# Optimization experiments

Hardware: AMD Instinct MI355X
Metric: run time of the kernel (lower is better)

## Reference

```python
import jax, jax.numpy as jnp
import numpy as np

HEADS = 16
DIM_HEAD = 64
SCALE = DIM_HEAD ** -0.5


def setup_inputs() -> dict:
    key = jax.random.key(0)
    k1, k2, k3, k4 = jax.random.split(key, 4)
    dim = 1024
    inner = HEADS * DIM_HEAD  # 1024
    b, n = 4, 2048
    x = jax.random.normal(k1, (b, n, dim), dtype=jnp.float32)
    # weights stored as [in, out] (equivalent math to torch Linear)
    w_qkv = jax.random.normal(k2, (dim, inner * 3), dtype=jnp.float32) * (dim ** -0.5)
    w_out = jax.random.normal(k3, (inner, dim), dtype=jnp.float32) * (inner ** -0.5)
    b_out = jax.random.normal(k4, (dim,), dtype=jnp.float32) * 0.01
    return {"x": x, "w_qkv": w_qkv, "w_out": w_out, "b_out": b_out}


def reference(x, w_qkv, w_out, b_out):
    b, n, dim = x.shape
    qkv = x @ w_qkv                                   # [b, n, 3*inner]
    q, k, v = jnp.split(qkv, 3, axis=-1)
    def to_heads(t):
        return t.reshape(b, n, HEADS, DIM_HEAD).transpose(0, 2, 1, 3)  # b h n d
    q, k, v = to_heads(q) * SCALE, to_heads(k), to_heads(v)
    dots = jnp.einsum('bhid,bhjd->bhij', q, k)        # [b, h, n, n]
    mask_value = -jnp.finfo(dots.dtype).max
    causal_mask = jnp.triu(jnp.ones((n, n), dtype=bool), k=1)
    dots = jnp.where(causal_mask, mask_value, dots)
    attn = jax.nn.softmax(dots, axis=-1)
    out = jnp.einsum('bhij,bhjd->bhid', attn, v)      # [b, h, n, d]
    out = out.transpose(0, 2, 1, 3).reshape(b, n, HEADS * DIM_HEAD)
    return out @ w_out + b_out
```

## Files before the change

kernel.cpp:

```cpp
#include <hip/hip_runtime.h>
#include <hip/hip_bf16.h>
#include <stdint.h>

typedef __attribute__((ext_vector_type(8))) short bf16x8;
typedef __attribute__((ext_vector_type(4))) float f32x4;
typedef __attribute__((ext_vector_type(4))) unsigned int uint32x4;

#define TOKENS 8192
#define DMODEL 1024
#define NQKV   3072
#define NSEQ   2048
#define NHEAD  16
#define DHEAD  64

__device__ __forceinline__ ushort f32_bf16(float f) {
    uint32_t u = __builtin_bit_cast(uint32_t, f);
    u = (u + 0x7fffu + ((u >> 16) & 1u)) >> 16;
    return (ushort)u;
}

__device__ __forceinline__ unsigned int cvt_pk_bf16(float lo, float hi) {
    unsigned int r;
    asm("v_cvt_pk_bf16_f32 %0, %1, %2" : "=v"(r) : "v"(lo), "v"(hi));
    return r;
}
__device__ __forceinline__ void permlane32_swap(unsigned int& a, unsigned int& b) {
    asm("v_permlane32_swap_b32 %0, %1" : "+v"(a), "+v"(b));
}
__device__ __forceinline__ void permlane16_swap(unsigned int& a, unsigned int& b) {
    asm("v_permlane16_swap_b32 %0, %1" : "+v"(a), "+v"(b));
}
__device__ __forceinline__ unsigned opaque_copy(unsigned x) {
    unsigned y;
    asm("v_mov_b32 %0, %1" : "=v"(y) : "v"(x));
    return y;
}

__device__ __forceinline__ float red_max_g(float x) {
    unsigned a = __builtin_bit_cast(unsigned, x);
    unsigned b = opaque_copy(a);
    permlane16_swap(a, b);
    float r = fmaxf(__builtin_bit_cast(float, a), __builtin_bit_cast(float, b));
    unsigned c = __builtin_bit_cast(unsigned, r);
    unsigned d = opaque_copy(c);
    permlane32_swap(c, d);
    return fmaxf(__builtin_bit_cast(float, c), __builtin_bit_cast(float, d));
}
__device__ __forceinline__ float red_sum_g(float x) {
    unsigned a = __builtin_bit_cast(unsigned, x);
    unsigned b = opaque_copy(a);
    permlane16_swap(a, b);
    float r = __builtin_bit_cast(float, a) + __builtin_bit_cast(float, b);
    unsigned c = __builtin_bit_cast(unsigned, r);
    unsigned d = opaque_copy(c);
    permlane32_swap(c, d);
    return __builtin_bit_cast(float, c) + __builtin_bit_cast(float, d);
}

__device__ __forceinline__ void gload16(const void* g, void* l) {
    __builtin_amdgcn_global_load_lds(
        (const __attribute__((address_space(1))) void*)g,
        (__attribute__((address_space(3))) void*)l, 16, 0, 0);
}

__device__ __forceinline__ void barf() {
    asm volatile("" ::: "memory");
    __builtin_amdgcn_s_barrier();
    asm volatile("" ::: "memory");
}

__global__ __launch_bounds__(256) void fused_cvt_kernel(
    const float* __restrict__ x,     ushort* __restrict__ xb,
    const float* __restrict__ wqkv,  ushort* __restrict__ wqkv_t,
    const float* __restrict__ wout,  ushort* __restrict__ wout_t)
{
    __shared__ float tile[64][65];
    const int bid = blockIdx.x;
    const int tid = threadIdx.x;

    if (bid < 8192) {
        const int i = bid * 256 + tid;
        float4 v = reinterpret_cast<const float4*>(x)[i];
        ushort4 o;
        o.x = f32_bf16(v.x); o.y = f32_bf16(v.y);
        o.z = f32_bf16(v.z); o.w = f32_bf16(v.w);
        reinterpret_cast<ushort4*>(xb)[i] = o;
        return;
    }

    const float* w; ushort* wt; int N, bx, by;
    if (bid < 8960) {
        const int r = bid - 8192;
        w = wqkv; wt = wqkv_t; N = NQKV;
        bx = r % 48; by = r / 48;
    } else {
        const int r = bid - 8960;
        w = wout; wt = wout_t; N = DMODEL;
        bx = r % 16; by = r / 16;
    }
    const int rr = tid >> 4;
    const int c4 = (tid & 15) * 4;
    const int n0 = bx * 64;
    const int k0 = by * 64;
    #pragma unroll
    for (int i = 0; i < 4; ++i) {
        const float4 v = *reinterpret_cast<const float4*>(&w[(size_t)(k0 + rr + i * 16) * N + n0 + c4]);
        tile[rr + i * 16][c4 + 0] = v.x;
        tile[rr + i * 16][c4 + 1] = v.y;
        tile[rr + i * 16][c4 + 2] = v.z;
        tile[rr + i * 16][c4 + 3] = v.w;
    }
    __syncthreads();
    #pragma unroll
    for (int i = 0; i < 4; ++i) {
        ushort4 o;
        o.x = f32_bf16(tile[c4 + 0][rr + i * 16]);
        o.y = f32_bf16(tile[c4 + 1][rr + i * 16]);
        o.z = f32_bf16(tile[c4 + 2][rr + i * 16]);
        o.w = f32_bf16(tile[c4 + 3][rr + i * 16]);
        *reinterpret_cast<ushort4*>(&wt[(size_t)(n0 + rr + i * 16) * 1024 + k0 + c4]) = o;
    }
}

template<int MODE, int NX>
__global__ __launch_bounds__(256) void gemm_bt(
    const ushort* __restrict__ A, const ushort* __restrict__ Bt,
    ushort* __restrict__ Qb, ushort* __restrict__ Kb, ushort* __restrict__ Vtb,
    float* __restrict__ Out, const float* __restrict__ bias)
{
    constexpr int K = 1024;
    __shared__ __align__(16) ushort As[2][128 * 32];
    __shared__ __align__(16) ushort Bs[2][128 * 32];

    const int lane = threadIdx.x & 63;
    const int w    = threadIdx.x >> 6;
    const int l16  = lane & 15;
    const int g    = lane >> 4;

    const int nwg  = (int)gridDim.x;
    const int chunk = nwg >> 3;
    const int swz  = (blockIdx.x & 7) * chunk + ((int)blockIdx.x >> 3);
    const int row0 = (swz / NX) * 128;
    const int col0 = (swz % NX) * 128;

    const int wr   = (w >> 1) * 64;
    const int wc   = (w & 1) * 64;

    const int srow  = w * 16 + (lane >> 2);
    const int sswz8 = ((lane & 3) ^ ((lane >> 3) & 3)) * 8;
    const ushort* Ag = A  + (size_t)(row0 + srow) * K + sswz8;
    const ushort* Bg = Bt + (size_t)(col0 + srow) * K + sswz8;
    const int woff = w * (16 * 32);

    const int cq8 = (g ^ ((l16 >> 1) & 3)) * 8;

    f32x4 acc[4][4] = {};

#define GSTAGE(BUF, KK) do {                                             \
        gload16(Ag + (KK),          &As[BUF][woff]);                     \
        gload16(Ag + 64 * K + (KK), &As[BUF][woff + 64 * 32]);           \
        gload16(Bg + (KK),          &Bs[BUF][woff]);                     \
        gload16(Bg + 64 * K + (KK), &Bs[BUF][woff + 64 * 32]);           \
    } while (0)

#define GCOMPUTE(BUF) do {                                               \
        bf16x8 a[4], b[4];                                               \
        _Pragma("unroll")                                                \
        for (int m = 0; m < 4; ++m)                                      \
            a[m] = *reinterpret_cast<const bf16x8*>(                     \
                &As[BUF][(wr + m * 16 + l16) * 32 + cq8]);               \
        _Pragma("unroll")                                                \
        for (int n = 0; n < 4; ++n)                                      \
            b[n] = *reinterpret_cast<const bf16x8*>(                     \
                &Bs[BUF][(wc + n * 16 + l16) * 32 + cq8]);               \
        _Pragma("unroll")                                                \
        for (int m = 0; m < 4; ++m)                                      \
            _Pragma("unroll")                                            \
            for (int n = 0; n < 4; ++n)                                  \
                acc[m][n] = __builtin_amdgcn_mfma_f32_16x16x32_bf16(     \
                    a[m], b[n], acc[m][n], 0, 0, 0);                     \
    } while (0)

    GSTAGE(0, 0);
    GSTAGE(1, 32);
    for (int kk = 0; kk + 128 <= K; kk += 64) {
        asm volatile("s_waitcnt vmcnt(4)" ::: "memory");
        barf();
        GCOMPUTE(0);
        barf();
        GSTAGE(0, kk + 64);
        asm volatile("s_waitcnt vmcnt(4)" ::: "memory");
        barf();
        GCOMPUTE(1);
        barf();
        GSTAGE(1, kk + 96);
    }
    asm volatile("s_waitcnt vmcnt(4)" ::: "memory");
    barf();
    GCOMPUTE(0);
    asm volatile("s_waitcnt vmcnt(0)" ::: "memory");
    barf();
    GCOMPUTE(1);
#undef GSTAGE
#undef GCOMPUTE

    if (MODE == 0) {
        const int part = col0 >> 10;
        const float QSC = 0.18033688011112042f;
        #pragma unroll
        for (int m = 0; m < 4; ++m) {
            const int trow = row0 + wr + m * 16 + 4 * g;
            #pragma unroll
            for (int n = 0; n < 4; ++n) {
                const int c  = col0 + wc + n * 16 + l16;
                const int cc = c & 1023;
                const int h  = cc >> 6, d = cc & 63;
                #pragma unroll
                for (int jj = 0; jj < 4; ++jj) {
                    const int t  = trow + jj;
                    const int bb = t >> 11, nn = t & 2047;
                    const float v = acc[m][n][jj];
                    const size_t bhid = (size_t)(bb * NHEAD + h);
                    if (part == 0)
                        Qb[(bhid * NSEQ + nn) * DHEAD + d] = f32_bf16(v * QSC);
                    else if (part == 1)
                        Kb[(bhid * NSEQ + nn) * DHEAD + d] = f32_bf16(v);
                    else
                        Vtb[bhid * (NSEQ * DHEAD) + (size_t)(nn >> 5) * (DHEAD * 32)
                            + d * 32 + (nn & 31)] = f32_bf16(v);
                }
            }
        }
    } else {
        #pragma unroll
        for (int m = 0; m < 4; ++m) {
            const int trow = row0 + wr + m * 16 + 4 * g;
            #pragma unroll
            for (int n = 0; n < 4; ++n) {
                const int c = col0 + wc + n * 16 + l16;
                const float bv = bias[c];
                #pragma unroll
                for (int jj = 0; jj < 4; ++jj)
                    Out[(size_t)(trow + jj) * DMODEL + c] = acc[m][n][jj] + bv;
            }
        }
    }
}

__device__ __forceinline__ void attn_qk(
    int kt, int qr0s, int l16, int g,
    const bf16x8 (&kk)[4][2],
    const bf16x8 qf0, const bf16x8 qf1,
    f32x4 (&oacc)[4], float& mrun, float& lsum,
    bf16x8& pf0, bf16x8& pf1)
{
    const f32x4 zero = {};
    f32x4 s[4];
    __builtin_amdgcn_s_setprio(1);
    #pragma unroll
    for (int t = 0; t < 4; ++t) {
        s[t] = __builtin_amdgcn_mfma_f32_16x16x32_bf16(kk[t][0], qf0, zero, 0, 0, 0);
        s[t] = __builtin_amdgcn_mfma_f32_16x16x32_bf16(kk[t][1], qf1, s[t], 0, 0, 0);
    }
    __builtin_amdgcn_s_setprio(0);
    if (kt + 63 > qr0s) {
        const int kb = kt + 4 * g - (qr0s + l16);
        #pragma unroll
        for (int t = 0; t < 4; ++t)
            #pragma unroll
            for (int jj = 0; jj < 4; ++jj)
                if (kb + 16 * t + jj > 0) s[t][jj] = -1e30f;
    }
    const float m0 = fmaxf(fmaxf(s[0][0], s[0][1]), s[0][2]);
    const float m1 = fmaxf(fmaxf(s[0][3], s[1][0]), s[1][1]);
    const float m2 = fmaxf(fmaxf(s[1][2], s[1][3]), s[2][0]);
    const float m3 = fmaxf(fmaxf(s[2][1], s[2][2]), s[2][3]);
    const float m4 = fmaxf(fmaxf(s[3][0], s[3][1]), s[3][2]);
    const float m5 = fmaxf(fmaxf(m0, m1), m2);
    const float m6 = fmaxf(fmaxf(m3, m4), s[3][3]);
    const float mxl = fmaxf(m5, m6);
    if (__any(mxl > mrun + 8.0f)) {
        const float mx = red_max_g(mxl);
        const float mn = fmaxf(mrun, mx);
        const float sc = __builtin_amdgcn_exp2f(mrun - mn);
        mrun = mn;
        lsum *= sc;
        float scj[4];
        #pragma unroll
        for (int jj = 0; jj < 4; ++jj) scj[jj] = __shfl(sc, 4 * g + jj);
        #pragma unroll
        for (int dt = 0; dt < 4; ++dt)
            #pragma unroll
            for (int jj = 0; jj < 4; ++jj) oacc[dt][jj] *= scj[jj];
    }
    float ps = 0.f;
    unsigned int pw[4][2];
    #pragma unroll
    for (int t = 0; t < 4; ++t) {
        const float p0 = __builtin_amdgcn_exp2f(s[t][0] - mrun);
        const float p1 = __builtin_amdgcn_exp2f(s[t][1] - mrun);
        const float p2 = __builtin_amdgcn_exp2f(s[t][2] - mrun);
        const float p3 = __builtin_amdgcn_exp2f(s[t][3] - mrun);
        ps += (p0 + p1) + (p2 + p3);
        pw[t][0] = cvt_pk_bf16(p0, p1);
        pw[t][1] = cvt_pk_bf16(p2, p3);
    }
    lsum += ps;
    unsigned int a0 = pw[0][0], a1 = pw[0][1], b0 = pw[1][0], b1 = pw[1][1];
    permlane32_swap(a0, b0); permlane32_swap(a1, b1);
    permlane16_swap(a0, b0); permlane16_swap(a1, b1);
    pf0 = __builtin_bit_cast(bf16x8, (uint32x4){a0, a1, b0, b1});
    unsigned int c0 = pw[2][0], c1 = pw[2][1], d0 = pw[3][0], d1 = pw[3][1];
    permlane32_swap(c0, d0); permlane32_swap(c1, d1);
    permlane16_swap(c0, d0); permlane16_swap(c1, d1);
    pf1 = __builtin_bit_cast(bf16x8, (uint32x4){c0, c1, d0, d1});
}

__global__ __launch_bounds__(256) void attn_kernel(
    const ushort* __restrict__ Qb, const ushort* __restrict__ Kb,
    const ushort* __restrict__ Vt, ushort* __restrict__ Ob)
{
    __shared__ __align__(16) ushort Klds[2][4096];
    __shared__ __align__(16) ushort Vlds[2][4096];

    const int lane = threadIdx.x & 63;
    const int w    = threadIdx.x >> 6;
    const int l16  = lane & 15;
    const int g    = lane >> 4;

    const int bid = blockIdx.x;
    const int xcd = bid & 7, ii = bid >> 3;
    const int bh  = xcd * 8 + (ii >> 4);
    const int jlo = ii & 15;
    const int jhi = 31 - jlo;

    const int qr0_lo = jlo * 64 + w * 16;
    const int qr0_hi = jhi * 64 + w * 16;
    const int nt = jhi + 1;

    const ushort* QpL = Qb + ((size_t)bh * NSEQ + qr0_lo + l16) * DHEAD + 8 * g;
    const ushort* QpH = Qb + ((size_t)bh * NSEQ + qr0_hi + l16) * DHEAD + 8 * g;
    const bf16x8 qfL0 = *reinterpret_cast<const bf16x8*>(QpL);
    const bf16x8 qfL1 = *reinterpret_cast<const bf16x8*>(QpL + 32);
    const bf16x8 qfH0 = *reinterpret_cast<const bf16x8*>(QpH);
    const bf16x8 qfH1 = *reinterpret_cast<const bf16x8*>(QpH + 32);

    const ushort* Kg = Kb + (size_t)bh * (NSEQ * DHEAD);
    const ushort* Vg = Vt + (size_t)bh * (NSEQ * DHEAD);

    const int q0    = w * 2;
    const int srow  = lane >> 2;
    const int sswz8 = ((lane & 3) ^ ((lane >> 3) & 3)) * 8;
    const int cq8   = (g ^ ((l16 >> 1) & 3)) * 8;

    f32x4 oaccL[4] = {}, oaccH[4] = {};
    float mrunL = -1e30f, lsumL = 0.f, mrunH = -1e30f, lsumH = 0.f;

    #pragma unroll
    for (int i = 0; i < 2; ++i) {
        const int q = q0 + i;
        gload16(Kg + (size_t)((q & 3) * 16 + srow) * 64 + (q >> 2) * 32 + sswz8,
                &Klds[0][q * 512]);
        gload16(Vg + (size_t)(q >> 2) * 2048 + ((q & 3) * 16 + srow) * 32 + sswz8,
                &Vlds[0][q * 512]);
    }
    __syncthreads();

    for (int t = 0; t < nt; ++t) {
        const int cur = t & 1;
        if (t + 1 < nt) {
            const int kt1 = (t + 1) * 64;
            #pragma unroll
            for (int i = 0; i < 2; ++i) {
                const int q = q0 + i;
                gload16(Kg + (size_t)(kt1 + (q & 3) * 16 + srow) * 64 + (q >> 2) * 32 + sswz8,
                        &Klds[cur ^ 1][q * 512]);
                gload16(Vg + (size_t)kt1 * 64 + (q >> 2) * 2048 + ((q & 3) * 16 + srow) * 32 + sswz8,
                        &Vlds[cur ^ 1][q * 512]);
            }
        }
        const int kt = t * 64;
        bf16x8 kk[4][2];
        #pragma unroll
        for (int tt = 0; tt < 4; ++tt) {
            #pragma unroll
            for (int h = 0; h < 2; ++h)
                kk[tt][h] = *reinterpret_cast<const bf16x8*>(
                    &Klds[cur][h * 2048 + (16 * tt + l16) * 32 + cq8]);
        }
        bf16x8 pfH0, pfH1, pfL0, pfL1;
        attn_qk(kt, qr0_hi, l16, g, kk, qfH0, qfH1, oaccH, mrunH, lsumH, pfH0, pfH1);
        const bool doLo = (t <= jlo);
        if (doLo)
            attn_qk(kt, qr0_lo, l16, g, kk, qfL0, qfL1, oaccL, mrunL, lsumL, pfL0, pfL1);
        __builtin_amdgcn_s_setprio(1);
        #pragma unroll
        for (int dt = 0; dt < 4; ++dt) {
            const bf16x8 v0 = *reinterpret_cast<const bf16x8*>(
                &Vlds[cur][(dt * 16 + l16) * 32 + cq8]);
            const bf16x8 v1 = *reinterpret_cast<const bf16x8*>(
                &Vlds[cur][2048 + (dt * 16 + l16) * 32 + cq8]);
            oaccH[dt] = __builtin_amdgcn_mfma_f32_16x16x32_bf16(pfH0, v0, oaccH[dt], 0, 0, 0);
            oaccH[dt] = __builtin_amdgcn_mfma_f32_16x16x32_bf16(pfH1, v1, oaccH[dt], 0, 0, 0);
            if (doLo) {
                oaccL[dt] = __builtin_amdgcn_mfma_f32_16x16x32_bf16(pfL0, v0, oaccL[dt], 0, 0, 0);
                oaccL[dt] = __builtin_amdgcn_mfma_f32_16x16x32_bf16(pfL1, v1, oaccL[dt], 0, 0, 0);
            }
        }
        __builtin_amdgcn_s_setprio(0);
        __syncthreads();
    }

    const int bb = bh >> 4, h = bh & 15;
    {
        const float inv = 1.0f / red_sum_g(lsumH);
        float invj[4];
        #pragma unroll
        for (int jj = 0; jj < 4; ++jj) invj[jj] = __shfl(inv, 4 * g + jj);
        #pragma unroll
        for (int jj = 0; jj < 4; ++jj) {
            const size_t t = (size_t)bb * NSEQ + qr0_hi + 4 * g + jj;
            #pragma unroll
            for (int dt = 0; dt < 4; ++dt)
                Ob[t * DMODEL + h * DHEAD + dt * 16 + l16] = f32_bf16(oaccH[dt][jj] * invj[jj]);
        }
    }
    {
        const float inv = 1.0f / red_sum_g(lsumL);
        float invj[4];
        #pragma unroll
        for (int jj = 0; jj < 4; ++jj) invj[jj] = __shfl(inv, 4 * g + jj);
        #pragma unroll
        for (int jj = 0; jj < 4; ++jj) {
            const size_t t = (size_t)bb * NSEQ + qr0_lo + 4 * g + jj;
            #pragma unroll
            for (int dt = 0; dt < 4; ++dt)
                Ob[t * DMODEL + h * DHEAD + dt * 16 + l16] = f32_bf16(oaccL[dt][jj] * invj[jj]);
        }
    }
}

extern "C" void kernel_launch(void* const* d_in, const int* in_sizes, int n_in,
                              void* d_out, int out_size, void* d_ws, size_t ws_size,
                              hipStream_t stream)
{
    const float* x     = (const float*)d_in[0];
    const float* w_qkv = (const float*)d_in[1];
    const float* w_out = (const float*)d_in[2];
    const float* b_out = (const float*)d_in[3];
    float* out = (float*)d_out;

    char* ws = (char*)d_ws;
    ushort* x_bf   = (ushort*)(ws);
    ushort* wqkv_t = (ushort*)(ws + 16777216);
    ushort* wout_t = (ushort*)(ws + 23068672);
    ushort* q_bf   = (ushort*)(ws + 25165824);
    ushort* k_bf   = (ushort*)(ws + 41943040);
    ushort* vt_bf  = (ushort*)(ws + 58720256);
    ushort* attn_bf = x_bf;

    fused_cvt_kernel<<<dim3(9216), dim3(256), 0, stream>>>(
        x, x_bf, w_qkv, wqkv_t, w_out, wout_t);

    gemm_bt<0, NQKV / 128><<<dim3((NQKV / 128) * (TOKENS / 128)), dim3(256), 0, stream>>>(
        x_bf, wqkv_t, q_bf, k_bf, vt_bf, nullptr, nullptr);

    attn_kernel<<<dim3(1024), dim3(256), 0, stream>>>(q_bf, k_bf, vt_bf, attn_bf);

    gemm_bt<1, DMODEL / 128><<<dim3((DMODEL / 128) * (TOKENS / 128)), dim3(256), 0, stream>>>(
        attn_bf, wout_t, nullptr, nullptr, nullptr, out, b_out);
}
```

Before: 205.7 us.

## Replace 4-wave GEMM with single-wave 64x64 tiles and barrier-free triple buffering

Result: slower. 242.7 us (+18.0%).

```diff
diff --git a/kernel.cpp b/kernel.cpp
--- a/kernel.cpp
+++ b/kernel.cpp
@@ -123,96 +123,92 @@
 }
 
 template<int MODE, int NX>
-__global__ __launch_bounds__(256) void gemm_bt(
+__global__ __launch_bounds__(64) void gemm_wp(
     const ushort* __restrict__ A, const ushort* __restrict__ Bt,
     ushort* __restrict__ Qb, ushort* __restrict__ Kb, ushort* __restrict__ Vtb,
     float* __restrict__ Out, const float* __restrict__ bias)
 {
     constexpr int K = 1024;
-    __shared__ __align__(16) ushort As[2][128 * 32];
-    __shared__ __align__(16) ushort Bs[2][128 * 32];
-
-    const int lane = threadIdx.x & 63;
-    const int w    = threadIdx.x >> 6;
+    __shared__ __align__(16) ushort As[3][64 * 32];
+    __shared__ __align__(16) ushort Bs[3][64 * 32];
+
+    const int lane = threadIdx.x;
     const int l16  = lane & 15;
     const int g    = lane >> 4;
 
-    const int nwg  = (int)gridDim.x;
+    const int nwg   = (int)gridDim.x;
     const int chunk = nwg >> 3;
-    const int swz  = (blockIdx.x & 7) * chunk + ((int)blockIdx.x >> 3);
-    const int row0 = (swz / NX) * 128;
-    const int col0 = (swz % NX) * 128;
-
-    const int wr   = (w >> 1) * 64;
-    const int wc   = (w & 1) * 64;
-
-    const int srow  = w * 16 + (lane >> 2);
+    const int swz   = (blockIdx.x & 7) * chunk + ((int)blockIdx.x >> 3);
+    const int row0  = (swz / NX) * 64;
+    const int col0  = (swz % NX) * 64;
+
+    const int srow  = lane >> 2;
     const int sswz8 = ((lane & 3) ^ ((lane >> 3) & 3)) * 8;
     const ushort* Ag = A  + (size_t)(row0 + srow) * K + sswz8;
     const ushort* Bg = Bt + (size_t)(col0 + srow) * K + sswz8;
-    const int woff = w * (16 * 32);
 
     const int cq8 = (g ^ ((l16 >> 1) & 3)) * 8;
 
     f32x4 acc[4][4] = {};
 
-#define GSTAGE(BUF, KK) do {                                             \
-        gload16(Ag + (KK),          &As[BUF][woff]);                     \
-        gload16(Ag + 64 * K + (KK), &As[BUF][woff + 64 * 32]);           \
-        gload16(Bg + (KK),          &Bs[BUF][woff]);                     \
-        gload16(Bg + 64 * K + (KK), &Bs[BUF][woff + 64 * 32]);           \
+#define WSTAGE(T) do { const int _b = (T) % 3; const int _k = (T) * 32;  \
+        gload16(Ag + _k,           &As[_b][0]);                          \
+        gload16(Ag + 16 * K + _k,  &As[_b][512]);                        \
+        gload16(Ag + 32 * K + _k,  &As[_b][1024]);                       \
+        gload16(Ag + 48 * K + _k,  &As[_b][1536]);                       \
+        gload16(Bg + _k,           &Bs[_b][0]);                          \
+        gload16(Bg + 16 * K + _k,  &Bs[_b][512]);                        \
+        gload16(Bg + 32 * K + _k,  &Bs[_b][1024]);                       \
+        gload16(Bg + 48 * K + _k,  &Bs[_b][1536]);                       \
     } while (0)
 
-#define GCOMPUTE(BUF) do {                                               \
+#define WBODY(T, DOSTAGE) do {                                           \
+        const int _buf = (T) % 3;                                        \
         bf16x8 a[4], b[4];                                               \
         _Pragma("unroll")                                                \
         for (int m = 0; m < 4; ++m)                                      \
             a[m] = *reinterpret_cast<const bf16x8*>(                     \
-                &As[BUF][(wr + m * 16 + l16) * 32 + cq8]);               \
+                &As[_buf][(m * 16 + l16) * 32 + cq8]);                   \
         _Pragma("unroll")                                                \
         for (int n = 0; n < 4; ++n)                                      \
             b[n] = *reinterpret_cast<const bf16x8*>(                     \
-                &Bs[BUF][(wc + n * 16 + l16) * 32 + cq8]);               \
+                &Bs[_buf][(n * 16 + l16) * 32 + cq8]);                   \
+        asm volatile("s_waitcnt lgkmcnt(0)" ::: "memory");               \
+        __builtin_amdgcn_sched_barrier(0);                               \
+        if (DOSTAGE) WSTAGE((T) + 3);                                    \
+        __builtin_amdgcn_s_setprio(1);                                   \
         _Pragma("unroll")                                                \
         for (int m = 0; m < 4; ++m)                                      \
             _Pragma("unroll")                                            \
             for (int n = 0; n < 4; ++n)                                  \
                 acc[m][n] = __builtin_amdgcn_mfma_f32_16x16x32_bf16(     \
                     a[m], b[n], acc[m][n], 0, 0, 0);                     \
+        __builtin_amdgcn_s_setprio(0);                                   \
     } while (0)
 
-    GSTAGE(0, 0);
-    GSTAGE(1, 32);
-    for (int kk = 0; kk + 128 <= K; kk += 64) {
-        asm volatile("s_waitcnt vmcnt(4)" ::: "memory");
-        barf();
-        GCOMPUTE(0);
-        barf();
-        GSTAGE(0, kk + 64);
-        asm volatile("s_waitcnt vmcnt(4)" ::: "memory");
-        barf();
-        GCOMPUTE(1);
-        barf();
-        GSTAGE(1, kk + 96);
-    }
-    asm volatile("s_waitcnt vmcnt(4)" ::: "memory");
-    barf();
-    GCOMPUTE(0);
+    WSTAGE(0); WSTAGE(1); WSTAGE(2);
+    for (int t = 0; t < 29; ++t) {
+        asm volatile("s_waitcnt vmcnt(16)" ::: "memory");
+        WBODY(t, true);
+    }
+    asm volatile("s_waitcnt vmcnt(16)" ::: "memory");
+    WBODY(29, false);
+    asm volatile("s_waitcnt vmcnt(8)" ::: "memory");
+    WBODY(30, false);
     asm volatile("s_waitcnt vmcnt(0)" ::: "memory");
-    barf();
-    GCOMPUTE(1);
-#undef GSTAGE
-#undef GCOMPUTE
+    WBODY(31, false);
+#undef WSTAGE
+#undef WBODY
 
     if (MODE == 0) {
         const int part = col0 >> 10;
         const float QSC = 0.18033688011112042f;
         #pragma unroll
         for (int m = 0; m < 4; ++m) {
-            const int trow = row0 + wr + m * 16 + 4 * g;
+            const int trow = row0 + m * 16 + 4 * g;
             #pragma unroll
             for (int n = 0; n < 4; ++n) {
-                const int c  = col0 + wc + n * 16 + l16;
+                const int c  = col0 + n * 16 + l16;
                 const int cc = c & 1023;
                 const int h  = cc >> 6, d = cc & 63;
                 #pragma unroll
@@ -234,10 +230,10 @@
     } else {
         #pragma unroll
         for (int m = 0; m < 4; ++m) {
-            const int trow = row0 + wr + m * 16 + 4 * g;
+            const int trow = row0 + m * 16 + 4 * g;
             #pragma unroll
             for (int n = 0; n < 4; ++n) {
-                const int c = col0 + wc + n * 16 + l16;
+                const int c = col0 + n * 16 + l16;
                 const float bv = bias[c];
                 #pragma unroll
                 for (int jj = 0; jj < 4; ++jj)
@@ -462,11 +458,11 @@
     fused_cvt_kernel<<<dim3(9216), dim3(256), 0, stream>>>(
         x, x_bf, w_qkv, wqkv_t, w_out, wout_t);
 
-    gemm_bt<0, NQKV / 128><<<dim3((NQKV / 128) * (TOKENS / 128)), dim3(256), 0, stream>>>(
+    gemm_wp<0, NQKV / 64><<<dim3((NQKV / 64) * (TOKENS / 64)), dim3(64), 0, stream>>>(
         x_bf, wqkv_t, q_bf, k_bf, vt_bf, nullptr, nullptr);
 
     attn_kernel<<<dim3(1024), dim3(256), 0, stream>>>(q_bf, k_bf, vt_bf, attn_bf);
 
-    gemm_bt<1, DMODEL / 128><<<dim3((DMODEL / 128) * (TOKENS / 128)), dim3(256), 0, stream>>>(
+    gemm_wp<1, DMODEL / 64><<<dim3((DMODEL / 64) * (TOKENS / 64)), dim3(64), 0, stream>>>(
         attn_bf, wout_t, nullptr, nullptr, nullptr, out, b_out);
 }
```
